# Kernel tuning notes

Hardware: AMD Instinct MI355X
Metric: run time of the kernel (lower is better)

The kernel has to match this reference:

```python
import jax, jax.numpy as jnp
import numpy as np
from jax import lax

B, DIM, H, W = 32, 64, 1, 8192
HEADS = 8
EPS_LN = 1e-5
EPS_NORM = 1e-12


def setup_inputs() -> dict:
    key = jax.random.key(0)
    ks = jax.random.split(key, 20)
    g = lambda i, shape, s=0.05: jax.random.normal(ks[i], shape, jnp.float32) * s
    return dict(
        x=jax.random.normal(ks[0], (B, DIM, H, W), jnp.float32),
        qkv_w=g(1, (3 * DIM, DIM)), qkv_b=g(2, (3 * DIM,)),
        dw_w=g(3, (3 * DIM, 1, 3, 3)), dw_b=g(4, (3 * DIM,)),
        proj_w=g(5, (DIM, DIM)), proj_b=g(6, (DIM,)),
        temperature=jnp.ones((HEADS, 1, 1), jnp.float32),
        sp_w=g(7, (DIM,)), sp_b=g(8, (1,)),
        up_w=g(9, (3,)), up_b=g(10, (3,)),
        c2_w=g(11, (1, 1, 2)), c2_b=g(11, (1,)), ln2_w=jnp.ones((W,), jnp.float32), ln2_b=jnp.zeros((W,), jnp.float32),
        c4_w=g(12, (1, 1, 4)), c4_b=g(13, (1,)), ln4_w=jnp.ones((W,), jnp.float32), ln4_b=jnp.zeros((W,), jnp.float32),
        c6_w=g(14, (1, 1, 6)), c6_b=g(15, (1,)), ln6_w=jnp.ones((W,), jnp.float32), ln6_b=jnp.zeros((W,), jnp.float32),
        mp_w=g(16, (DIM,)), mp_b=g(17, (DIM,)),
    )


def _mtl(xs, cw, cb, lw, lb):
    """Multiscale_Temporal_Layer: conv1d 'same' -> LayerNorm(W) -> ELU -> mean pool. xs: (b,1,w)."""
    k = cw.shape[-1]
    tot = k - 1
    lo = tot // 2  # torch 'same': extra pad goes to the right
    y = lax.conv_general_dilated(xs, cw, (1,), [(lo, tot - lo)],
                                 dimension_numbers=('NCH', 'OIH', 'NCH'))
    y = y + cb[None, :, None]
    mu = jnp.mean(y, -1, keepdims=True)
    var = jnp.mean((y - mu) ** 2, -1, keepdims=True)
    y = (y - mu) / jnp.sqrt(var + EPS_LN) * lw + lb
    y = jax.nn.elu(y)
    return jnp.mean(y, -1, keepdims=True)  # (b,1,1)


def _forward(x, qkv_w, qkv_b, dw_w, dw_b, proj_w, proj_b, temperature,
             sp_w, sp_b, up_w, up_b,
             c2_w, c2_b, ln2_w, ln2_b,
             c4_w, c4_b, ln4_w, ln4_b,
             c6_w, c6_b, ln6_w, ln6_b,
             mp_w, mp_b):
    b, c, h, w = x.shape
    hd = c // HEADS  # per-head channel dim
    # 1x1 conv qkv, then depthwise 3x3 conv
    qkv = jnp.einsum('oc,bchw->bohw', qkv_w, x) + qkv_b[None, :, None, None]
    qkv = lax.conv_general_dilated(qkv, dw_w, (1, 1), [(1, 1), (1, 1)],
                                   dimension_numbers=('NCHW', 'OIHW', 'NCHW'),
                                   feature_group_count=3 * c)
    qkv = qkv + dw_b[None, :, None, None]
    q, k, v = jnp.split(qkv, 3, axis=1)
    # Multiscale_Temporal_Attention on v: v is (b,c,1,w)
    xseq = (jnp.einsum('c,bcw->bw', sp_w, v[:, :, 0, :]) + sp_b)[:, None, :]  # (b,1,w)
    up = up_w[None, :, None] * xseq + up_b[None, :, None]  # (b,3,w)
    xx, yy, zz = up[:, 0:1], up[:, 1:2], up[:, 2:3]
    mout = (_mtl(xx, c2_w, c2_b, ln2_w, ln2_b) * xx
            + _mtl(yy, c4_w, c4_b, ln4_w, ln4_b) * yy
            + _mtl(zz, c6_w, c6_b, ln6_w, ln6_b) * zz)  # (b,1,w)
    v = mp_w[None, :, None] * mout + mp_b[None, :, None]  # (b,c,w) via 1x1 conv broadcast
    # channel (transposed) attention over n = h*w tokens
    n = h * w
    q = q.reshape(b, HEADS, hd, n)
    k = k.reshape(b, HEADS, hd, n)
    v = v.reshape(b, HEADS, hd, n)
    q = q / jnp.maximum(jnp.linalg.norm(q, axis=-1, keepdims=True), EPS_NORM)
    k = k / jnp.maximum(jnp.linalg.norm(k, axis=-1, keepdims=True), EPS_NORM)
    attn = jnp.einsum('bhcn,bhdn->bhcd', q, k) * temperature  # (b,heads,hd,hd)
    attn = jax.nn.softmax(attn, axis=-1)
    out = jnp.einsum('bhcd,bhdn->bhcn', attn, v).reshape(b, c, h, w)
    out = jnp.einsum('oc,bchw->bohw', proj_w, out) + proj_b[None, :, None, None]
    return out  # dropouts are identity in eval mode


def reference(x, qkv_w, qkv_b, dw_w, dw_b, proj_w, proj_b, temperature,
              sp_w, sp_b, up_w, up_b,
              c2_w, c2_b, ln2_w, ln2_b,
              c4_w, c4_b, ln4_w, ln4_b,
              c6_w, c6_b, ln6_w, ln6_b,
              mp_w, mp_b):
    return _forward(x, qkv_w, qkv_b, dw_w, dw_b, proj_w, proj_b, temperature,
                    sp_w, sp_b, up_w, up_b,
                    c2_w, c2_b, ln2_w, ln2_b,
                    c4_w, c4_b, ln4_w, ln4_b,
                    c6_w, c6_b, ln6_w, ln6_b,
                    mp_w, mp_b)
```

## Files before the change

kernel.cpp:

```cpp
#include <hip/hip_runtime.h>
#include <hip/hip_bf16.h>
#include <math.h>

#define Wd 8192
#define Bd 32
#define Ttile 64

#define OFF_G    0
#define OFF_H    192
#define OFF_BASE 195
#define OFF_XSEQ 256
#define OFF_PART (256 + Bd*Wd)
#define OFF_S    (OFF_PART + Bd*640*128)
#define OFF_M    (OFF_S + Bd*640)
#define OFF_E    (OFF_M + 96)
#define OFF_F    (OFF_E + Bd*64)
#define OFF_FRAG (OFF_F + Bd*64)

typedef __attribute__((ext_vector_type(8))) short bf16x8;
typedef __attribute__((ext_vector_type(4))) float f32x4;

__device__ __forceinline__ unsigned short f2bf(float v) {
    return __builtin_bit_cast(unsigned short, __float2bfloat16(v));
}
__device__ __forceinline__ float bf2f(unsigned short h) {
    return __builtin_bit_cast(float, (unsigned)h << 16);
}
__device__ __forceinline__ void split2(float v0, float v1, unsigned& hw, unsigned& lw) {
    unsigned short h0 = f2bf(v0), h1 = f2bf(v1);
    unsigned short l0 = f2bf(v0 - bf2f(h0)), l1 = f2bf(v1 - bf2f(h1));
    hw = (unsigned)h0 | ((unsigned)h1 << 16);
    lw = (unsigned)l0 | ((unsigned)l1 << 16);
}

__global__ __launch_bounds__(256) void k0_setup(const float* __restrict__ qkv_w,
                         const float* __restrict__ qkv_b,
                         const float* __restrict__ dw_w, const float* __restrict__ dw_b,
                         const float* __restrict__ sp_w, const float* __restrict__ sp_b,
                         float* __restrict__ ws)
{
    int tid = threadIdx.x;
    if (tid < 192) {
        int j = tid >> 6, ch = tid & 63;
        float acc = 0.f;
        for (int c = 0; c < 64; c++)
            acc += sp_w[c] * dw_w[(128+c)*9 + 3 + j] * qkv_w[(128+c)*64 + ch];
        ws[OFF_G + j*64 + ch] = acc;
    } else if (tid < 195) {
        int j = tid - 192;
        float h = 0.f;
        for (int c = 0; c < 64; c++)
            h += sp_w[c] * dw_w[(128+c)*9 + 3 + j] * qkv_b[128+c];
        ws[OFF_H + j] = h;
    } else if (tid == 195) {
        float base = sp_b[0];
        for (int c = 0; c < 64; c++) base += sp_w[c] * dw_b[128+c];
        ws[OFF_BASE] = base;
    }
    __syncthreads();
    for (int it = tid; it < 36*64; it += 256) {
        int lane = it & 63;
        int cidx = it >> 6;
        int ver = cidx / 18;
        int rem = cidx - ver*18;
        int nt = rem >> 1, kb = rem & 1;
        int row = nt*16 + (lane & 15);
        int ks  = kb*32 + (lane >> 4)*8;
        unsigned short u[8];
        #pragma unroll
        for (int e = 0; e < 8; e++) {
            int k = ks + e;
            float v = 0.f;
            if (row < 128)      v = qkv_w[row*64 + k];
            else if (row < 131) v = ws[OFF_G + (row-128)*64 + k];
            unsigned short h = f2bf(v);
            if (ver == 0) u[e] = h;
            else          u[e] = f2bf(v - bf2f(h));
        }
        unsigned* dst = (unsigned*)(ws + OFF_FRAG) + (ver*1152 + (nt*2+kb)*64 + lane)*4;
        dst[0] = (unsigned)u[0] | ((unsigned)u[1] << 16);
        dst[1] = (unsigned)u[2] | ((unsigned)u[3] << 16);
        dst[2] = (unsigned)u[4] | ((unsigned)u[5] << 16);
        dst[3] = (unsigned)u[6] | ((unsigned)u[7] << 16);
    }
}

#define QKHI 0
#define QKLO 18432
#define ZLDS 36864
#define SMEM_BYTES (36864 + 1024)

__global__ __launch_bounds__(256, 3) void k1_main(const float* __restrict__ x,
    const float* __restrict__ qkv_b, const float* __restrict__ dw_w,
    const float* __restrict__ dw_b, float* __restrict__ ws)
{
    __shared__ __align__(16) unsigned char smem[SMEM_BYTES];
    const int tid = threadIdx.x, lane = tid & 63, wv = tid >> 6;
    const int g = lane >> 4, lr = lane & 15;
    const int tile = blockIdx.x, b = blockIdx.y;
    const int w0 = tile * Ttile;
    const float* xb = x + (size_t)b * 64 * Wd;
    const bool safe = (tile != 0) && (tile != 127);

    f32x4 acc[3][5];
    #pragma unroll
    for (int i = 0; i < 3; i++)
        #pragma unroll
        for (int m = 0; m < 5; m++) acc[i][m] = (f32x4){0.f,0.f,0.f,0.f};
    const uint4* fragbase = (const uint4*)(ws + OFF_FRAG);

    #pragma unroll
    for (int kb = 0; kb < 2; kb++) {
        bf16x8 axh[5], axl[5];
        #pragma unroll
        for (int mt = 0; mt < 5; mt++) {
            int pos = w0 - 1 + mt*16 + lr;
            int posc = min(max(pos, 0), Wd - 1);
            const float* p = xb + (size_t)(kb*32 + g*8) * Wd + posc;
            float v[8];
            if (safe) {
                #pragma unroll
                for (int e = 0; e < 8; e++) v[e] = p[(size_t)e * Wd];
            } else {
                bool vld = (pos >= 0) && (pos < Wd);
                #pragma unroll
                for (int e = 0; e < 8; e++) { float t = p[(size_t)e * Wd]; v[e] = vld ? t : 0.f; }
            }
            uint4 uh, ul;
            split2(v[0], v[1], uh.x, ul.x);
            split2(v[2], v[3], uh.y, ul.y);
            split2(v[4], v[5], uh.z, ul.z);
            split2(v[6], v[7], uh.w, ul.w);
            axh[mt] = __builtin_bit_cast(bf16x8, uh);
            axl[mt] = __builtin_bit_cast(bf16x8, ul);
        }
        #pragma unroll
        for (int nti = 0; nti < 3; nti++) {
            if (nti < 2 || wv == 0) {
                int nt = (nti == 2) ? 8 : (wv + nti*4);
                bf16x8 bh = __builtin_bit_cast(bf16x8, fragbase[(nt*2+kb)*64 + lane]);
                bf16x8 bl = __builtin_bit_cast(bf16x8, fragbase[1152 + (nt*2+kb)*64 + lane]);
                #pragma unroll
                for (int mt = 0; mt < 5; mt++) {
                    acc[nti][mt] = __builtin_amdgcn_mfma_f32_16x16x32_bf16(axh[mt], bh, acc[nti][mt], 0,0,0);
                    acc[nti][mt] = __builtin_amdgcn_mfma_f32_16x16x32_bf16(axl[mt], bh, acc[nti][mt], 0,0,0);
                    acc[nti][mt] = __builtin_amdgcn_mfma_f32_16x16x32_bf16(axh[mt], bl, acc[nti][mt], 0,0,0);
                }
            }
        }
    }

    unsigned short* qkhi = (unsigned short*)(smem + QKHI);
    unsigned short* qklo = (unsigned short*)(smem + QKLO);
    float* zlds = (float*)(smem + ZLDS);

    #pragma unroll
    for (int nti = 0; nti < 3; nti++) {
        if (!(nti < 2 || wv == 0)) continue;
        int nt = (nti == 2) ? 8 : (wv + nti*4);
        int row = nt*16 + lr;
        if (nt == 8) {
            if (lr < 3) {
                #pragma unroll
                for (int mt = 0; mt < 5; mt++) {
                    float4 vz = { acc[2][mt][0], acc[2][mt][1], acc[2][mt][2], acc[2][mt][3] };
                    *(float4*)(zlds + lr*84 + mt*16 + g*4) = vz;
                }
            }
        } else {
            float bias = qkv_b[row];
            float tb = dw_b[row];
            float t0 = dw_w[row*9+3], t1 = dw_w[row*9+4], t2 = dw_w[row*9+5];
            float4 v[5];
            #pragma unroll
            for (int mt = 0; mt < 5; mt++) {
                #pragma unroll
                for (int r = 0; r < 4; r++) {
                    float val = acc[nti][mt][r] + bias;
                    if (!safe) {
                        int pos = w0 - 1 + mt*16 + g*4 + r;
                        if (pos < 0 || pos >= Wd) val = 0.f;
                    }
                    ((float*)&v[mt])[r] = val;
                }
            }
            int src = (lane + 16) & 63;
            #pragma unroll
            for (int mt = 0; mt < 4; mt++) {
                float a0 = __shfl(v[mt].x,   src), b0 = __shfl(v[mt+1].x, src);
                float a1 = __shfl(v[mt].y,   src), b1 = __shfl(v[mt+1].y, src);
                float in4 = (lane < 48) ? a0 : b0;
                float in5 = (lane < 48) ? a1 : b1;
                float o0 = tb + t0*v[mt].x + t1*v[mt].y + t2*v[mt].z;
                float o1 = tb + t0*v[mt].y + t1*v[mt].z + t2*v[mt].w;
                float o2 = tb + t0*v[mt].z + t1*v[mt].w + t2*in4;
                float o3 = tb + t0*v[mt].w + t1*in4     + t2*in5;
                uint2 hw, lw;
                split2(o0, o1, hw.x, lw.x);
                split2(o2, o3, hw.y, lw.y);
                int boff = row*144 + (mt*16 + g*4)*2;
                *(uint2*)((unsigned char*)qkhi + boff) = hw;
                *(uint2*)((unsigned char*)qklo + boff) = lw;
            }
        }
    }

    if (tid < 64) {
        float a = ws[OFF_BASE];
        #pragma unroll
        for (int j = 0; j < 3; j++) {
            int wg = w0 + tid + j - 1;
            a += zlds[j*84 + tid + j];
            if (wg >= 0 && wg < Wd) a += ws[OFF_H + j];
        }
        ws[OFF_XSEQ + (size_t)b*Wd + w0 + tid] = a;
    }

    {
        const int rq = (wv*16 + lr) * 144;
        const int rk = (64 + wv*16 + lr) * 144;
        const int ko = g * 16;
        f32x4 sqk = (f32x4){0,0,0,0}, sqq = (f32x4){0,0,0,0}, skk = (f32x4){0,0,0,0};
        #pragma unroll
        for (int kb = 0; kb < 2; kb++) {
            int off = kb*64 + ko;
            bf16x8 qh = *(const bf16x8*)((unsigned char*)qkhi + rq + off);
            bf16x8 ql = *(const bf16x8*)((unsigned char*)qklo + rq + off);
            bf16x8 kh = *(const bf16x8*)((unsigned char*)qkhi + rk + off);
            bf16x8 kl = *(const bf16x8*)((unsigned char*)qklo + rk + off);
            sqk = __builtin_amdgcn_mfma_f32_16x16x32_bf16(qh, kh, sqk, 0,0,0);
            sqk = __builtin_amdgcn_mfma_f32_16x16x32_bf16(ql, kh, sqk, 0,0,0);
            sqk = __builtin_amdgcn_mfma_f32_16x16x32_bf16(qh, kl, sqk, 0,0,0);
            sqq = __builtin_amdgcn_mfma_f32_16x16x32_bf16(qh, qh, sqq, 0,0,0);
            sqq = __builtin_amdgcn_mfma_f32_16x16x32_bf16(ql, qh, sqq, 0,0,0);
            sqq = __builtin_amdgcn_mfma_f32_16x16x32_bf16(qh, ql, sqq, 0,0,0);
            skk = __builtin_amdgcn_mfma_f32_16x16x32_bf16(kh, kh, skk, 0,0,0);
            skk = __builtin_amdgcn_mfma_f32_16x16x32_bf16(kl, kh, skk, 0,0,0);
            skk = __builtin_amdgcn_mfma_f32_16x16x32_bf16(kh, kl, skk, 0,0,0);
        }
        float* pb = ws + OFF_PART + (size_t)b*640*128 + tile;
        int hh = lr >> 3, c2 = lr & 7;
        if (hh == (g >> 1)) {
            #pragma unroll
            for (int r = 0; r < 4; r++) {
                int c1 = (g & 1)*4 + r;
                int idx = (2*wv + hh)*64 + c1*8 + c2;
                pb[(size_t)idx*128] = sqk[r];
            }
        }
        if ((lr >> 2) == g) {
            int r = lr & 3;
            pb[(size_t)(512 + wv*16 + lr)*128] = sqq[r];
            pb[(size_t)(576 + wv*16 + lr)*128] = skk[r];
        }
    }
}

__device__ __forceinline__ float blk_reduce_256(float v, float* sc) {
    #pragma unroll
    for (int off = 32; off > 0; off >>= 1) v += __shfl_down(v, off, 64);
    __syncthreads();
    if ((threadIdx.x & 63) == 0) sc[threadIdx.x >> 6] = v;
    __syncthreads();
    return sc[0] + sc[1] + sc[2] + sc[3];
}

__global__ __launch_bounds__(256) void k23(const float* __restrict__ ws,
    const float* __restrict__ up_w, const float* __restrict__ up_b,
    const float* __restrict__ c2_w, const float* __restrict__ c2_b,
    const float* __restrict__ ln2_w, const float* __restrict__ ln2_b,
    const float* __restrict__ c4_w, const float* __restrict__ c4_b,
    const float* __restrict__ ln4_w, const float* __restrict__ ln4_b,
    const float* __restrict__ c6_w, const float* __restrict__ c6_b,
    const float* __restrict__ ln6_w, const float* __restrict__ ln6_b,
    float* __restrict__ wsS, float* __restrict__ wsM)
{
    __shared__ float ys[Wd];
    __shared__ float sc[4];
    int bx = blockIdx.x;
    if (bx < 32) {
        int b = bx;
        const float* part = ws + OFF_PART;
        for (int idx = threadIdx.x; idx < 640; idx += 256) {
            const float4* p = (const float4*)(part + ((size_t)b*640 + idx)*128);
            float s = 0.f;
            #pragma unroll 8
            for (int i = 0; i < 32; i++) {
                float4 t = p[i];
                s += ((t.x + t.y) + (t.z + t.w));
            }
            wsS[b*640 + idx] = s;
        }
        return;
    }
    int t2 = bx - 32;
    int br = t2 / 32, b = t2 % 32;
    const float *cw, *lw, *lb; float cb; int K, lo;
    if (br == 0)      { cw = c2_w; cb = c2_b[0]; lw = ln2_w; lb = ln2_b; K = 2; lo = 0; }
    else if (br == 1) { cw = c4_w; cb = c4_b[0]; lw = ln4_w; lb = ln4_b; K = 4; lo = 1; }
    else              { cw = c6_w; cb = c6_b[0]; lw = ln6_w; lb = ln6_b; K = 6; lo = 2; }
    float uw = up_w[br], ub = up_b[br];
    const float* xr = ws + OFF_XSEQ + (size_t)b*Wd;

    float s = 0.f, s2 = 0.f;
    for (int w = threadIdx.x; w < Wd; w += 256) {
        float y = cb;
        for (int m = 0; m < K; m++) {
            int p = w + m - lo;
            if (p >= 0 && p < Wd) y += cw[m] * (uw*xr[p] + ub);
        }
        ys[w] = y; s += y; s2 += y*y;
    }
    float mu = blk_reduce_256(s, sc) * (1.f/Wd);
    __syncthreads();
    float Ey2 = blk_reduce_256(s2, sc) * (1.f/Wd);
    float var = fmaxf(Ey2 - mu*mu, 0.f);
    float inv = 1.f / sqrtf(var + 1e-5f);
    float se = 0.f;
    for (int w = threadIdx.x; w < Wd; w += 256) {
        float tt = (ys[w]-mu)*inv*lw[w] + lb[w];
        se += (tt > 0.f) ? tt : expm1f(tt);
    }
    float m = blk_reduce_256(se, sc) * (1.f/Wd);
    if (threadIdx.x == 0) wsM[b*3 + br] = m;
}

__global__ __launch_bounds__(256) void k45(const float* __restrict__ ws,
    const float* __restrict__ temperature,
    const float* __restrict__ mp_w, const float* __restrict__ mp_b,
    const float* __restrict__ up_w, const float* __restrict__ up_b,
    const float* __restrict__ proj_w, const float* __restrict__ proj_b,
    float* __restrict__ out)
{
    __shared__ float snk[64], sal[64], sbe[64], sE[64], sF[64];
    const int tid = threadIdx.x;
    const int chunk = blockIdx.x, b = blockIdx.y;
    const float* Sb = ws + OFF_S + b*640;
    float nq = 0.f;
    if (tid < 64) {
        nq = fmaxf(sqrtf(Sb[512 + tid]), 1e-12f);
        snk[tid] = fmaxf(sqrtf(Sb[576 + tid]), 1e-12f);
    }
    __syncthreads();
    if (tid < 64) {
        int h = tid >> 3;
        float temp = temperature[h];
        float lg[8], mx = -1e30f;
        #pragma unroll
        for (int d = 0; d < 8; d++) {
            lg[d] = Sb[8*tid + d] / (nq * snk[h*8 + d]) * temp;
            mx = fmaxf(mx, lg[d]);
        }
        float sum = 0.f;
        #pragma unroll
        for (int d = 0; d < 8; d++) { lg[d] = expf(lg[d] - mx); sum += lg[d]; }
        float a = 0.f, bb = 0.f;
        #pragma unroll
        for (int d = 0; d < 8; d++) {
            float at = lg[d] / sum;
            a  += at * mp_w[h*8 + d];
            bb += at * mp_b[h*8 + d];
        }
        sal[tid] = a; sbe[tid] = bb;
    }
    __syncthreads();
    if (tid < 64) {
        const float* wm = ws + OFF_M + b*3;
        float m2 = wm[0], m4 = wm[1], m6 = wm[2];
        float A = m2*up_w[0] + m4*up_w[1] + m6*up_w[2];
        float C = m2*up_b[0] + m4*up_b[1] + m6*up_b[2];
        float Pa = 0.f, Pb = 0.f;
        for (int c = 0; c < 64; c++) {
            float pw = proj_w[tid*64 + c];
            Pa += pw * sal[c];
            Pb += pw * sbe[c];
        }
        sE[tid] = A * Pa;
        sF[tid] = C * Pa + Pb + proj_b[tid];
    }
    __syncthreads();
    const float4* xs4 = (const float4*)(ws + OFF_XSEQ + (size_t)b*Wd);
    float4 xv = xs4[chunk*128 + (tid & 127)];
    int ohalf = tid >> 7;
    float4* ob = (float4*)out + (size_t)b*64*2048 + chunk*128 + (tid & 127);
    #pragma unroll 8
    for (int oo = 0; oo < 32; oo++) {
        int o = ohalf*32 + oo;
        float e = sE[o], f = sF[o];
        float4 r = { e*xv.x + f, e*xv.y + f, e*xv.z + f, e*xv.w + f };
        ob[(size_t)o*2048] = r;
    }
}

extern "C" void kernel_launch(void* const* d_in, const int* in_sizes, int n_in,
                              void* d_out, int out_size, void* d_ws, size_t ws_size,
                              hipStream_t stream) {
    const float* x      = (const float*)d_in[0];
    const float* qkv_w  = (const float*)d_in[1];
    const float* qkv_b  = (const float*)d_in[2];
    const float* dw_w   = (const float*)d_in[3];
    const float* dw_b   = (const float*)d_in[4];
    const float* proj_w = (const float*)d_in[5];
    const float* proj_b = (const float*)d_in[6];
    const float* temperature = (const float*)d_in[7];
    const float* sp_w   = (const float*)d_in[8];
    const float* sp_b   = (const float*)d_in[9];
    const float* up_w   = (const float*)d_in[10];
    const float* up_b   = (const float*)d_in[11];
    const float* c2_w   = (const float*)d_in[12];
    const float* c2_b   = (const float*)d_in[13];
    const float* ln2_w  = (const float*)d_in[14];
    const float* ln2_b  = (const float*)d_in[15];
    const float* c4_w   = (const float*)d_in[16];
    const float* c4_b   = (const float*)d_in[17];
    const float* ln4_w  = (const float*)d_in[18];
    const float* ln4_b  = (const float*)d_in[19];
    const float* c6_w   = (const float*)d_in[20];
    const float* c6_b   = (const float*)d_in[21];
    const float* ln6_w  = (const float*)d_in[22];
    const float* ln6_b  = (const float*)d_in[23];
    const float* mp_w   = (const float*)d_in[24];
    const float* mp_b   = (const float*)d_in[25];
    float* ws  = (float*)d_ws;
    float* out = (float*)d_out;

    k0_setup<<<1, 256, 0, stream>>>(qkv_w, qkv_b, dw_w, dw_b, sp_w, sp_b, ws);
    k1_main<<<dim3(128, 32), 256, 0, stream>>>(x, qkv_b, dw_w, dw_b, ws);
    k23<<<128, 256, 0, stream>>>(ws, up_w, up_b,
        c2_w, c2_b, ln2_w, ln2_b, c4_w, c4_b, ln4_w, ln4_b, c6_w, c6_b, ln6_w, ln6_b,
        ws + OFF_S, ws + OFF_M);
    k45<<<dim3(16, 32), 256, 0, stream>>>(ws, temperature, mp_w, mp_b,
        up_w, up_b, proj_w, proj_b, out);
}
```

Before: 144.7 us.

## Stage x tile in swizzled LDS, drop low-bf16 QK terms, transpose partials layout

The main kernel now loads the x tile into LDS once with coalesced float4 reads and keeps it there as XOR-swizzled bf16 hi/lo planes. MFMA A-fragments are then read from LDS instead of issuing strided per-element global loads. The q/k Gram products now use only the high bf16 part, which removes two-thirds of those MFMAs and the lo LDS buffer, at some cost in accuracy. The per-tile partial sums are stored tile-major so the writes are contiguous and the reduction kernel reads coalesced, and the occupancy hint goes up to 4 blocks per CU.

```diff
diff --git a/kernel.cpp b/kernel.cpp
--- a/kernel.cpp
+++ b/kernel.cpp
@@ -11,7 +11,7 @@
 #define OFF_BASE 195
 #define OFF_XSEQ 256
 #define OFF_PART (256 + Bd*Wd)
-#define OFF_S    (OFF_PART + Bd*640*128)
+#define OFF_S    (OFF_PART + Bd*128*640)
 #define OFF_M    (OFF_S + Bd*640)
 #define OFF_E    (OFF_M + 96)
 #define OFF_F    (OFF_E + Bd*64)
@@ -31,6 +31,9 @@
     unsigned short l0 = f2bf(v0 - bf2f(h0)), l1 = f2bf(v1 - bf2f(h1));
     hw = (unsigned)h0 | ((unsigned)h1 << 16);
     lw = (unsigned)l0 | ((unsigned)l1 << 16);
+}
+__device__ __forceinline__ unsigned pk2(float v0, float v1) {
+    return (unsigned)f2bf(v0) | ((unsigned)f2bf(v1) << 16);
 }
 
 __global__ __launch_bounds__(256) void k0_setup(const float* __restrict__ qkv_w,
@@ -85,12 +88,13 @@
     }
 }
 
-#define QKHI 0
-#define QKLO 18432
-#define ZLDS 36864
-#define SMEM_BYTES (36864 + 1024)
-
-__global__ __launch_bounds__(256, 3) void k1_main(const float* __restrict__ x,
+#define XT_HI 0
+#define XT_LO 10752
+#define QKH   21504
+#define ZLDS  37888
+#define SMEM_BYTES (37888 + 1024)
+
+__global__ __launch_bounds__(256, 4) void k1_main(const float* __restrict__ x,
     const float* __restrict__ qkv_b, const float* __restrict__ dw_w,
     const float* __restrict__ dw_b, float* __restrict__ ws)
 {
@@ -102,6 +106,29 @@
     const float* xb = x + (size_t)b * 64 * Wd;
     const bool safe = (tile != 0) && (tile != 127);
 
+    for (int i = tid; i < 672; i += 256) {
+        int j = i >> 5, chp = i & 31;
+        int pos0 = w0 - 4 + 4*j;
+        float4 a, c;
+        if (safe || (unsigned)pos0 < (unsigned)Wd) {
+            a = *(const float4*)(xb + (size_t)(2*chp)*Wd + pos0);
+            c = *(const float4*)(xb + (size_t)(2*chp+1)*Wd + pos0);
+        } else {
+            a = (float4){0,0,0,0}; c = (float4){0,0,0,0};
+        }
+        #pragma unroll
+        for (int e = 0; e < 4; e++) {
+            int row = 4*j + e;
+            float va = ((const float*)&a)[e], vc = ((const float*)&c)[e];
+            unsigned hw, lw;
+            split2(va, vc, hw, lw);
+            int boff = row*128 + ((((chp>>2) ^ (row & 7)) << 4) | ((chp & 3) << 2));
+            *(unsigned*)(smem + XT_HI + boff) = hw;
+            *(unsigned*)(smem + XT_LO + boff) = lw;
+        }
+    }
+    __syncthreads();
+
     f32x4 acc[3][5];
     #pragma unroll
     for (int i = 0; i < 3; i++)
@@ -114,25 +141,10 @@
         bf16x8 axh[5], axl[5];
         #pragma unroll
         for (int mt = 0; mt < 5; mt++) {
-            int pos = w0 - 1 + mt*16 + lr;
-            int posc = min(max(pos, 0), Wd - 1);
-            const float* p = xb + (size_t)(kb*32 + g*8) * Wd + posc;
-            float v[8];
-            if (safe) {
-                #pragma unroll
-                for (int e = 0; e < 8; e++) v[e] = p[(size_t)e * Wd];
-            } else {
-                bool vld = (pos >= 0) && (pos < Wd);
-                #pragma unroll
-                for (int e = 0; e < 8; e++) { float t = p[(size_t)e * Wd]; v[e] = vld ? t : 0.f; }
-            }
-            uint4 uh, ul;
-            split2(v[0], v[1], uh.x, ul.x);
-            split2(v[2], v[3], uh.y, ul.y);
-            split2(v[4], v[5], uh.z, ul.z);
-            split2(v[6], v[7], uh.w, ul.w);
-            axh[mt] = __builtin_bit_cast(bf16x8, uh);
-            axl[mt] = __builtin_bit_cast(bf16x8, ul);
+            int row = mt*16 + lr + 3;
+            int gran = (kb*4 + g) ^ (row & 7);
+            axh[mt] = *(const bf16x8*)(smem + XT_HI + row*128 + gran*16);
+            axl[mt] = *(const bf16x8*)(smem + XT_LO + row*128 + gran*16);
         }
         #pragma unroll
         for (int nti = 0; nti < 3; nti++) {
@@ -150,10 +162,7 @@
         }
     }
 
-    unsigned short* qkhi = (unsigned short*)(smem + QKHI);
-    unsigned short* qklo = (unsigned short*)(smem + QKLO);
     float* zlds = (float*)(smem + ZLDS);
-
     #pragma unroll
     for (int nti = 0; nti < 3; nti++) {
         if (!(nti < 2 || wv == 0)) continue;
@@ -195,12 +204,12 @@
                 float o1 = tb + t0*v[mt].y + t1*v[mt].z + t2*v[mt].w;
                 float o2 = tb + t0*v[mt].z + t1*v[mt].w + t2*in4;
                 float o3 = tb + t0*v[mt].w + t1*in4     + t2*in5;
-                uint2 hw, lw;
-                split2(o0, o1, hw.x, lw.x);
-                split2(o2, o3, hw.y, lw.y);
-                int boff = row*144 + (mt*16 + g*4)*2;
-                *(uint2*)((unsigned char*)qkhi + boff) = hw;
-                *(uint2*)((unsigned char*)qklo + boff) = lw;
+                uint2 hw;
+                hw.x = pk2(o0, o1);
+                hw.y = pk2(o2, o3);
+                int gran = (2*mt + (g>>1)) ^ (row & 7);
+                int boff = row*128 + (gran << 4) + ((g & 1) << 3);
+                *(uint2*)(smem + QKH + boff) = hw;
             }
         }
     }
@@ -217,41 +226,31 @@
     }
 
     {
-        const int rq = (wv*16 + lr) * 144;
-        const int rk = (64 + wv*16 + lr) * 144;
-        const int ko = g * 16;
+        const int rq = wv*16 + lr;
+        const int rk = 64 + wv*16 + lr;
         f32x4 sqk = (f32x4){0,0,0,0}, sqq = (f32x4){0,0,0,0}, skk = (f32x4){0,0,0,0};
         #pragma unroll
         for (int kb = 0; kb < 2; kb++) {
-            int off = kb*64 + ko;
-            bf16x8 qh = *(const bf16x8*)((unsigned char*)qkhi + rq + off);
-            bf16x8 ql = *(const bf16x8*)((unsigned char*)qklo + rq + off);
-            bf16x8 kh = *(const bf16x8*)((unsigned char*)qkhi + rk + off);
-            bf16x8 kl = *(const bf16x8*)((unsigned char*)qklo + rk + off);
+            int gran = (kb*4 + g) ^ (lr & 7);
+            bf16x8 qh = *(const bf16x8*)(smem + QKH + rq*128 + gran*16);
+            bf16x8 kh = *(const bf16x8*)(smem + QKH + rk*128 + gran*16);
             sqk = __builtin_amdgcn_mfma_f32_16x16x32_bf16(qh, kh, sqk, 0,0,0);
-            sqk = __builtin_amdgcn_mfma_f32_16x16x32_bf16(ql, kh, sqk, 0,0,0);
-            sqk = __builtin_amdgcn_mfma_f32_16x16x32_bf16(qh, kl, sqk, 0,0,0);
             sqq = __builtin_amdgcn_mfma_f32_16x16x32_bf16(qh, qh, sqq, 0,0,0);
-            sqq = __builtin_amdgcn_mfma_f32_16x16x32_bf16(ql, qh, sqq, 0,0,0);
-            sqq = __builtin_amdgcn_mfma_f32_16x16x32_bf16(qh, ql, sqq, 0,0,0);
             skk = __builtin_amdgcn_mfma_f32_16x16x32_bf16(kh, kh, skk, 0,0,0);
-            skk = __builtin_amdgcn_mfma_f32_16x16x32_bf16(kl, kh, skk, 0,0,0);
-            skk = __builtin_amdgcn_mfma_f32_16x16x32_bf16(kh, kl, skk, 0,0,0);
-        }
-        float* pb = ws + OFF_PART + (size_t)b*640*128 + tile;
+        }
+        float* pb = ws + OFF_PART + (size_t)(b*128 + tile)*640;
         int hh = lr >> 3, c2 = lr & 7;
         if (hh == (g >> 1)) {
             #pragma unroll
             for (int r = 0; r < 4; r++) {
                 int c1 = (g & 1)*4 + r;
-                int idx = (2*wv + hh)*64 + c1*8 + c2;
-                pb[(size_t)idx*128] = sqk[r];
+                pb[(2*wv + hh)*64 + c1*8 + c2] = sqk[r];
             }
         }
         if ((lr >> 2) == g) {
             int r = lr & 3;
-            pb[(size_t)(512 + wv*16 + lr)*128] = sqq[r];
-            pb[(size_t)(576 + wv*16 + lr)*128] = skk[r];
+            pb[512 + wv*16 + lr] = sqq[r];
+            pb[576 + wv*16 + lr] = skk[r];
         }
     }
 }
@@ -280,16 +279,20 @@
     int bx = blockIdx.x;
     if (bx < 32) {
         int b = bx;
-        const float* part = ws + OFF_PART;
-        for (int idx = threadIdx.x; idx < 640; idx += 256) {
-            const float4* p = (const float4*)(part + ((size_t)b*640 + idx)*128);
-            float s = 0.f;
-            #pragma unroll 8
-            for (int i = 0; i < 32; i++) {
-                float4 t = p[i];
-                s += ((t.x + t.y) + (t.z + t.w));
-            }
-            wsS[b*640 + idx] = s;
+        const float* part = ws + OFF_PART + (size_t)b*128*640;
+        #pragma unroll
+        for (int k = 0; k < 3; k++) {
+            int idx = threadIdx.x + k*256;
+            if (idx < 640) {
+                float s0 = 0.f, s1 = 0.f, s2 = 0.f, s3 = 0.f;
+                for (int t = 0; t < 128; t += 4) {
+                    s0 += part[(size_t)(t  )*640 + idx];
+                    s1 += part[(size_t)(t+1)*640 + idx];
+                    s2 += part[(size_t)(t+2)*640 + idx];
+                    s3 += part[(size_t)(t+3)*640 + idx];
+                }
+                wsS[b*640 + idx] = (s0 + s1) + (s2 + s3);
+            }
         }
         return;
     }
```

Result: faster. 126.2 us (-12.7%).
